# Performance work log

Hardware: AMD Instinct MI355X
Metric: run time of the kernel (lower is better)

The kernel has to match this reference:

```python
import jax, jax.numpy as jnp
import numpy as np

B, S, H = 64, 4096, 512

def setup_inputs() -> dict:
    key = jax.random.key(0)
    ks = jax.random.split(key, 8)
    decoder_output = jax.random.normal(ks[0], (B, H), dtype=jnp.float32)
    encoder_output = jax.random.normal(ks[1], (B, S, 2 * H), dtype=jnp.float32)
    mask = jax.random.randint(ks[2], (B, S), 0, 2).astype(bool)
    mask = mask.at[:, 0].set(True)  # guarantee at least one valid position per row
    sc_h = 1.0 / np.sqrt(2 * H)
    sc_s = 1.0 / np.sqrt(H)
    W_h_w = jax.random.uniform(ks[3], (H, 2 * H), jnp.float32, -sc_h, sc_h)
    W_h_b = jax.random.uniform(ks[4], (H,), jnp.float32, -sc_h, sc_h)
    W_s_w = jax.random.uniform(ks[5], (H, H), jnp.float32, -sc_s, sc_s)
    W_s_b = jax.random.uniform(ks[6], (H,), jnp.float32, -sc_s, sc_s)
    v_w = jax.random.uniform(ks[7], (1, H), jnp.float32, -sc_s, sc_s)
    return {"decoder_output": decoder_output, "encoder_output": encoder_output,
            "mask": mask, "W_h_w": W_h_w, "W_h_b": W_h_b,
            "W_s_w": W_s_w, "W_s_b": W_s_b, "v_w": v_w}

def reference(decoder_output, encoder_output, mask, W_h_w, W_h_b, W_s_w, W_s_b, v_w):
    # enc proj: [B,S,H]; dec proj: [B,H] broadcast over S
    enc = jnp.einsum('bse,he->bsh', encoder_output, W_h_w) + W_h_b
    dec = decoder_output @ W_s_w.T + W_s_b  # [B,H]
    x = jnp.tanh(enc + dec[:, None, :])     # [B,S,H]
    scores = jnp.einsum('bsh,h->bs', x, v_w[0])  # [B,S]
    masked = jnp.where(mask, scores, -jnp.inf)
    return jax.nn.softmax(masked, axis=-1)
```

## Files before the change

kernel.cpp:

```cpp
#include <hip/hip_runtime.h>
#include <math.h>

typedef __attribute__((ext_vector_type(8))) short bf16x8;
typedef __attribute__((ext_vector_type(4))) float f32x4;
typedef __attribute__((ext_vector_type(4))) unsigned short u16x4;

#define NB 64
#define NS 4096
#define NH 512
#define NE 1024
#define APITCH 80

__device__ __forceinline__ unsigned short f2bf(float f) {
  unsigned int u = __float_as_uint(f);
  u += 0x7fffu + ((u >> 16) & 1u);
  return (unsigned short)(u >> 16);
}

__device__ __forceinline__ float fast_tanh(float x) {
  float e = __expf(2.0f * x);
  return 1.0f - 2.0f * __builtin_amdgcn_rcpf(e + 1.0f);
}

__global__ __launch_bounds__(256) void prep_b_kernel(const float* __restrict__ W,
                                                     unsigned short* __restrict__ Bp) {
  const int t = blockIdx.x * 256 + threadIdx.x;
  const int lane = t & 63;
  const int ni = (t >> 6) & 3;
  const int kb = (t >> 8) & 31;
  const int w = t >> 13;
  const int col = w * 64 + ni * 16 + (lane & 15);
  const int k0 = kb * 32 + (lane >> 4) * 8;
  const float* src = W + col * NE + k0;
  float4 a = *(const float4*)src;
  float4 b = *(const float4*)(src + 4);
  union { bf16x8 v; unsigned short u[8]; } p;
  p.u[0] = f2bf(a.x); p.u[1] = f2bf(a.y); p.u[2] = f2bf(a.z); p.u[3] = f2bf(a.w);
  p.u[4] = f2bf(b.x); p.u[5] = f2bf(b.y); p.u[6] = f2bf(b.z); p.u[7] = f2bf(b.w);
  *(bf16x8*)(Bp + (long long)t * 8) = p.v;
}

__global__ __launch_bounds__(512) void prep_dec_kernel(const float* __restrict__ dec,
                                                       const float* __restrict__ Wsw,
                                                       const float* __restrict__ Wsb,
                                                       const float* __restrict__ Whb,
                                                       float* __restrict__ decb) {
  int b = blockIdx.x;
  int h = threadIdx.x;
  const float4* dr = (const float4*)(dec + b * NH);
  const float4* wr = (const float4*)(Wsw + h * NH);
  float sum = Wsb[h] + Whb[h];
#pragma unroll 8
  for (int i = 0; i < NH / 4; ++i) {
    float4 a = dr[i], w = wr[i];
    sum += a.x * w.x + a.y * w.y + a.z * w.z + a.w * w.w;
  }
  decb[b * NH + h] = sum;
}

__global__ __launch_bounds__(512, 4) void fused_main(const float* __restrict__ enc,
                                                     const unsigned short* __restrict__ Bp,
                                                     const float* __restrict__ decb,
                                                     const float* __restrict__ vw,
                                                     float* __restrict__ scores) {
  __shared__ __align__(16) char As[2][64 * APITCH];
  __shared__ float ssc[64];

  const int tid = threadIdx.x;
  const int lane = tid & 63;
  const int wave = tid >> 6;
  const int r15 = lane & 15;
  const int c4 = lane >> 4;
  const long long m0 = (long long)blockIdx.x * 64;

  if (tid < 64) ssc[tid] = 0.0f;

  const int arow = tid >> 3;
  const int achk = tid & 7;
  const float* aload = enc + (m0 + arow) * NE + achk * 4;
  const int awr = arow * APITCH + achk * 8;

  const unsigned short* const bb = Bp + (long long)wave * 32 * 2048 + lane * 8;

  f32x4 acc[4][4];
#pragma unroll
  for (int mi = 0; mi < 4; ++mi)
#pragma unroll
    for (int ni = 0; ni < 4; ++ni) {
      f32x4 z = {0.f, 0.f, 0.f, 0.f};
      acc[mi][ni] = z;
    }

  bf16x8 bA[4], bB[4];
#pragma unroll
  for (int ni = 0; ni < 4; ++ni) bA[ni] = *(const bf16x8*)(bb + ni * 512);
  {
    float4 a0 = *(const float4*)(aload);
    unsigned int p0, p1;
    asm("v_cvt_pk_bf16_f32 %0, %1, %2" : "=v"(p0) : "v"(a0.x), "v"(a0.y));
    asm("v_cvt_pk_bf16_f32 %0, %1, %2" : "=v"(p1) : "v"(a0.z), "v"(a0.w));
    uint2 wv; wv.x = p0; wv.y = p1;
    *(uint2*)(&As[0][0] + awr) = wv;
  }
  float4 aCur = *(const float4*)(aload + 32);
  asm volatile("s_waitcnt lgkmcnt(0)" ::: "memory");
  __builtin_amdgcn_s_barrier();
  __builtin_amdgcn_sched_barrier(0);

#pragma unroll
  for (int t = 0; t < 32; ++t) {
    const char* Ab = &As[t & 1][0];
    const bf16x8* bpn = (const bf16x8*)(bb + (t + 1) * 2048);
    float4 aNew;
#pragma unroll
    for (int p = 0; p < 4; ++p) {
      if (p == 0 && t < 30) aNew = *(const float4*)(aload + (t + 2) * 32);
      if (t < 31) {
        if (t & 1) bA[p] = bpn[p * 64];
        else       bB[p] = bpn[p * 64];
      }
      bf16x8 af = *(const bf16x8*)(Ab + (p * 16 + r15) * APITCH + c4 * 16);
      __builtin_amdgcn_s_setprio(1);
#pragma unroll
      for (int ni = 0; ni < 4; ++ni)
        acc[p][ni] = __builtin_amdgcn_mfma_f32_16x16x32_bf16(
            af, (t & 1) ? bB[ni] : bA[ni], acc[p][ni], 0, 0, 0);
      __builtin_amdgcn_s_setprio(0);
      if (p == 3) {
        if (t < 31) {
          unsigned int w0, w1;
          asm("v_cvt_pk_bf16_f32 %0, %1, %2" : "=v"(w0) : "v"(aCur.x), "v"(aCur.y));
          asm("v_cvt_pk_bf16_f32 %0, %1, %2" : "=v"(w1) : "v"(aCur.z), "v"(aCur.w));
          uint2 wv; wv.x = w0; wv.y = w1;
          *(uint2*)(&As[(t & 1) ^ 1][0] + awr) = wv;
          aCur = aNew;
        }
        asm volatile("s_waitcnt lgkmcnt(0)" ::: "memory");
        __builtin_amdgcn_sched_barrier(0);
      }
      __builtin_amdgcn_s_barrier();
    }
  }

  const int bidx = (int)(m0 >> 12);
  const float* decrow = decb + bidx * NH;
  float part[4][4];
#pragma unroll
  for (int mi = 0; mi < 4; ++mi)
#pragma unroll
    for (int j = 0; j < 4; ++j) part[mi][j] = 0.f;

#pragma unroll
  for (int ni = 0; ni < 4; ++ni) {
    int col = (wave << 6) + ni * 16 + r15;
    float vc = vw[col];
    float dc = decrow[col];
#pragma unroll
    for (int mi = 0; mi < 4; ++mi)
#pragma unroll
      for (int j = 0; j < 4; ++j)
        part[mi][j] += vc * fast_tanh(acc[mi][ni][j] + dc);
  }
#pragma unroll
  for (int off = 1; off < 16; off <<= 1)
#pragma unroll
    for (int mi = 0; mi < 4; ++mi)
#pragma unroll
      for (int j = 0; j < 4; ++j)
        part[mi][j] += __shfl_xor(part[mi][j], off, 64);

  if (r15 == 0) {
#pragma unroll
    for (int mi = 0; mi < 4; ++mi)
#pragma unroll
      for (int j = 0; j < 4; ++j)
        atomicAdd(&ssc[mi * 16 + c4 * 4 + j], part[mi][j]);
  }
  __syncthreads();
  if (tid < 64) scores[m0 + tid] = ssc[tid];
}

__global__ __launch_bounds__(1024) void softmax_kernel(const float* __restrict__ scores,
                                                       const int* __restrict__ mask,
                                                       float* __restrict__ out) {
  __shared__ float rmax[16];
  __shared__ float rsum[16];
  const int b = blockIdx.x;
  const int t = threadIdx.x;
  const int wid = t >> 6;
  const int ln = t & 63;
  const int base = b * NS;

  float s[4];
  int mk[4];
  float mx = -INFINITY;
#pragma unroll
  for (int i = 0; i < 4; ++i) {
    int idx = t + i * 1024;
    s[i] = scores[base + idx];
    mk[i] = mask[base + idx];
    if (mk[i]) mx = fmaxf(mx, s[i]);
  }
#pragma unroll
  for (int off = 1; off < 64; off <<= 1) mx = fmaxf(mx, __shfl_xor(mx, off, 64));
  if (ln == 0) rmax[wid] = mx;
  __syncthreads();
  float m2 = -INFINITY;
#pragma unroll
  for (int i = 0; i < 16; ++i) m2 = fmaxf(m2, rmax[i]);

  float e[4];
  float sum = 0.f;
#pragma unroll
  for (int i = 0; i < 4; ++i) {
    e[i] = mk[i] ? expf(s[i] - m2) : 0.f;
    sum += e[i];
  }
#pragma unroll
  for (int off = 1; off < 64; off <<= 1) sum += __shfl_xor(sum, off, 64);
  if (ln == 0) rsum[wid] = sum;
  __syncthreads();
  float tot = 0.f;
#pragma unroll
  for (int i = 0; i < 16; ++i) tot += rsum[i];
  float inv = 1.0f / tot;
#pragma unroll
  for (int i = 0; i < 4; ++i) {
    int idx = t + i * 1024;
    out[base + idx] = e[i] * inv;
  }
}

extern "C" void kernel_launch(void* const* d_in, const int* in_sizes, int n_in,
                              void* d_out, int out_size, void* d_ws, size_t ws_size,
                              hipStream_t stream) {
  const float* dec = (const float*)d_in[0];
  const float* enc = (const float*)d_in[1];
  const int* mask = (const int*)d_in[2];
  const float* Whw = (const float*)d_in[3];
  const float* Whb = (const float*)d_in[4];
  const float* Wsw = (const float*)d_in[5];
  const float* Wsb = (const float*)d_in[6];
  const float* vw = (const float*)d_in[7];
  float* out = (float*)d_out;

  unsigned short* Bp = (unsigned short*)d_ws;
  float* decb = (float*)((char*)d_ws + (1 << 20));
  float* scoresb = (float*)((char*)d_ws + (1 << 20) + (128 << 10));

  prep_b_kernel<<<dim3(256), dim3(256), 0, stream>>>(Whw, Bp);
  prep_dec_kernel<<<dim3(64), dim3(512), 0, stream>>>(dec, Wsw, Wsb, Whb, decb);
  fused_main<<<dim3(4096), dim3(512), 0, stream>>>(enc, Bp, decb, vw, scoresb);
  softmax_kernel<<<dim3(64), dim3(1024), 0, stream>>>(scoresb, mask, out);
}
```

Measured before the change: 394.2 us.

## Restructure GEMM k-loop to one barrier per step with batched LDS reads

The k-loop previously hit a workgroup barrier after each of four sub-steps and interleaved its global and LDS loads with the MFMAs. It now issues all global loads for the next k-tile at the top of the step, reads the four A fragments from LDS at once, runs all 16 MFMAs, then writes the next A tile and takes a single barrier. This cuts barrier count fourfold but shortens the prefetch distance for A from two steps to one, so global-memory latency may be exposed more.

Result: slower. 435.7 us (+10.5%).

```diff
diff --git a/kernel.cpp b/kernel.cpp
--- a/kernel.cpp
+++ b/kernel.cpp
@@ -79,6 +79,7 @@
   const int achk = tid & 7;
   const float* aload = enc + (m0 + arow) * NE + achk * 4;
   const int awr = arow * APITCH + achk * 8;
+  const int rdb = r15 * APITCH + c4 * 16;
 
   const unsigned short* const bb = Bp + (long long)wave * 32 * 2048 + lane * 8;
 
@@ -91,55 +92,68 @@
       acc[mi][ni] = z;
     }
 
-  bf16x8 bA[4], bB[4];
-#pragma unroll
-  for (int ni = 0; ni < 4; ++ni) bA[ni] = *(const bf16x8*)(bb + ni * 512);
+  bf16x8 bEv[4], bOd[4];
+#pragma unroll
+  for (int ni = 0; ni < 4; ++ni) bEv[ni] = *(const bf16x8*)(bb + ni * 512);
   {
     float4 a0 = *(const float4*)(aload);
-    unsigned int p0, p1;
-    asm("v_cvt_pk_bf16_f32 %0, %1, %2" : "=v"(p0) : "v"(a0.x), "v"(a0.y));
-    asm("v_cvt_pk_bf16_f32 %0, %1, %2" : "=v"(p1) : "v"(a0.z), "v"(a0.w));
-    uint2 wv; wv.x = p0; wv.y = p1;
+    unsigned int w0, w1;
+    asm("v_cvt_pk_bf16_f32 %0, %1, %2" : "=v"(w0) : "v"(a0.x), "v"(a0.y));
+    asm("v_cvt_pk_bf16_f32 %0, %1, %2" : "=v"(w1) : "v"(a0.z), "v"(a0.w));
+    uint2 wv; wv.x = w0; wv.y = w1;
     *(uint2*)(&As[0][0] + awr) = wv;
   }
-  float4 aCur = *(const float4*)(aload + 32);
   asm volatile("s_waitcnt lgkmcnt(0)" ::: "memory");
   __builtin_amdgcn_s_barrier();
-  __builtin_amdgcn_sched_barrier(0);
 
 #pragma unroll
   for (int t = 0; t < 32; ++t) {
+    float4 aT;
+    if (t < 31) {
+      aT = *(const float4*)(aload + (t + 1) * 32);
+      const bf16x8* bp = (const bf16x8*)(bb + (t + 1) * 2048);
+      if (t & 1) {
+#pragma unroll
+        for (int ni = 0; ni < 4; ++ni) bEv[ni] = bp[ni * 64];
+      } else {
+#pragma unroll
+        for (int ni = 0; ni < 4; ++ni) bOd[ni] = bp[ni * 64];
+      }
+    }
     const char* Ab = &As[t & 1][0];
-    const bf16x8* bpn = (const bf16x8*)(bb + (t + 1) * 2048);
-    float4 aNew;
-#pragma unroll
-    for (int p = 0; p < 4; ++p) {
-      if (p == 0 && t < 30) aNew = *(const float4*)(aload + (t + 2) * 32);
-      if (t < 31) {
-        if (t & 1) bA[p] = bpn[p * 64];
-        else       bB[p] = bpn[p * 64];
-      }
-      bf16x8 af = *(const bf16x8*)(Ab + (p * 16 + r15) * APITCH + c4 * 16);
-      __builtin_amdgcn_s_setprio(1);
-#pragma unroll
-      for (int ni = 0; ni < 4; ++ni)
-        acc[p][ni] = __builtin_amdgcn_mfma_f32_16x16x32_bf16(
-            af, (t & 1) ? bB[ni] : bA[ni], acc[p][ni], 0, 0, 0);
-      __builtin_amdgcn_s_setprio(0);
-      if (p == 3) {
-        if (t < 31) {
-          unsigned int w0, w1;
-          asm("v_cvt_pk_bf16_f32 %0, %1, %2" : "=v"(w0) : "v"(aCur.x), "v"(aCur.y));
-          asm("v_cvt_pk_bf16_f32 %0, %1, %2" : "=v"(w1) : "v"(aCur.z), "v"(aCur.w));
-          uint2 wv; wv.x = w0; wv.y = w1;
-          *(uint2*)(&As[(t & 1) ^ 1][0] + awr) = wv;
-          aCur = aNew;
-        }
-        asm volatile("s_waitcnt lgkmcnt(0)" ::: "memory");
-        __builtin_amdgcn_sched_barrier(0);
-      }
-      __builtin_amdgcn_s_barrier();
+    bf16x8 af0 = *(const bf16x8*)(Ab + rdb);
+    bf16x8 af1 = *(const bf16x8*)(Ab + 16 * APITCH + rdb);
+    bf16x8 af2 = *(const bf16x8*)(Ab + 32 * APITCH + rdb);
+    bf16x8 af3 = *(const bf16x8*)(Ab + 48 * APITCH + rdb);
+    __builtin_amdgcn_sched_barrier(0);
+    __builtin_amdgcn_s_setprio(1);
+#pragma unroll
+    for (int ni = 0; ni < 4; ++ni)
+      acc[0][ni] = __builtin_amdgcn_mfma_f32_16x16x32_bf16(
+          af0, (t & 1) ? bOd[ni] : bEv[ni], acc[0][ni], 0, 0, 0);
+#pragma unroll
+    for (int ni = 0; ni < 4; ++ni)
+      acc[1][ni] = __builtin_amdgcn_mfma_f32_16x16x32_bf16(
+          af1, (t & 1) ? bOd[ni] : bEv[ni], acc[1][ni], 0, 0, 0);
+#pragma unroll
+    for (int ni = 0; ni < 4; ++ni)
+      acc[2][ni] = __builtin_amdgcn_mfma_f32_16x16x32_bf16(
+          af2, (t & 1) ? bOd[ni] : bEv[ni], acc[2][ni], 0, 0, 0);
+#pragma unroll
+    for (int ni = 0; ni < 4; ++ni)
+      acc[3][ni] = __builtin_amdgcn_mfma_f32_16x16x32_bf16(
+          af3, (t & 1) ? bOd[ni] : bEv[ni], acc[3][ni], 0, 0, 0);
+    __builtin_amdgcn_s_setprio(0);
+    if (t < 31) {
+      unsigned int w0, w1;
+      asm("v_cvt_pk_bf16_f32 %0, %1, %2" : "=v"(w0) : "v"(aT.x), "v"(aT.y));
+      asm("v_cvt_pk_bf16_f32 %0, %1, %2" : "=v"(w1) : "v"(aT.z), "v"(aT.w));
+      uint2 wv; wv.x = w0; wv.y = w1;
+      *(uint2*)(&As[(t + 1) & 1][0] + awr) = wv;
     }
+    asm volatile("s_waitcnt lgkmcnt(0)" ::: "memory");
+    __builtin_amdgcn_sched_barrier(0);
+    __builtin_amdgcn_s_barrier();
   }
 
   const int bidx = (int)(m0 >> 12);
```
